# Kernel optimization log

Hardware: AMD Instinct MI355X
Metric: run time of the kernel (lower is better)

## Reference

```python
import jax, jax.numpy as jnp
import numpy as np

N, E = 30000, 180000
IN, H, OUT = 3000, 512, 30


def _segment_softmax(e, dst, n):
    # numerically stable softmax over incoming edges of each destination node
    m = jax.ops.segment_max(e, dst, num_segments=n)
    m = jnp.where(jnp.isfinite(m), m, 0.0)  # nodes with no in-edges
    ex = jnp.exp(e - m[dst])
    den = jax.ops.segment_sum(ex, dst, num_segments=n)
    return ex / den[dst]


def _gat(x, src, dst, Ws, Wd, a_s, a_d, n, alpha=None):
    """edGATConv (heads=1, no self-loops, no bias).
    xs = lin_s(x); attention score from lin_s(x)[src] and lin_d(x)[dst];
    out[i] = sum_{e: dst_e=i} alpha_e * xs[src_e].
    If alpha is given (tie_alpha), reuse it instead of recomputing."""
    xs = x @ Ws.T  # [n, F_out]
    if alpha is None:
        xd = x @ Wd.T
        e = jax.nn.leaky_relu(xs[src] @ a_s + xd[dst] @ a_d, 0.2)  # [E]
        alpha = _segment_softmax(e, dst, n)
    out = jax.ops.segment_sum(alpha[:, None] * xs[src], dst, num_segments=n)
    return out, alpha


def setup_inputs() -> dict:
    key = jax.random.key(0)
    ks = jax.random.split(key, 7)
    features = jax.random.normal(ks[0], (N, IN), dtype=jnp.float32)
    edge_index = jax.random.randint(ks[1], (2, E), 0, N)
    W1s = jax.random.normal(ks[2], (H, IN), dtype=jnp.float32) * 0.02
    W1d = jax.random.normal(ks[3], (H, IN), dtype=jnp.float32) * 0.02
    a1s = jax.random.normal(ks[4], (H,), dtype=jnp.float32) * 0.1
    a1d = jax.random.normal(ks[5], (H,), dtype=jnp.float32) * 0.1
    W2s = jax.random.normal(ks[6], (OUT, H), dtype=jnp.float32) * 0.05
    return {"features": features, "edge_index": edge_index,
            "W1s": W1s, "W1d": W1d, "a1s": a1s, "a1d": a1d, "W2s": W2s}


def reference(features, edge_index, W1s, W1d, a1s, a1d, W2s):
    src, dst = edge_index[0], edge_index[1]
    n = features.shape[0]
    # conv1: attentive GAT layer, stores tie_alpha
    h1, alpha1 = _gat(features, src, dst, W1s, W1d, a1s, a1d, n)
    h1 = jax.nn.elu(h1)
    # conv2: aslinear=True -> plain linear with lin_s
    h2 = h1 @ W2s.T  # [N, OUT]
    # conv3: weights tied to conv2 transposed, alpha tied to conv1
    # W3s = W2s.T so xs3 = h2 @ W3s.T = h2 @ W2s
    h3, _ = _gat(h2, src, dst, W2s.T, None, None, None, n, alpha=alpha1)
    h3 = jax.nn.elu(h3)
    # conv4: aslinear, weight tied to conv1 transposed: h3 @ W4s.T = h3 @ W1s
    h4 = h3 @ W1s  # [N, IN]
    return (h2, h4)
```

## Files before the change

kernel.cpp:

```cpp
#include <hip/hip_runtime.h>

typedef unsigned short u16;
typedef __bf16 bf16_t;
typedef bf16_t bf16x8 __attribute__((ext_vector_type(8)));
typedef float f32x4 __attribute__((ext_vector_type(4)));
typedef u16 u16x8 __attribute__((ext_vector_type(8)));

#define AS1 __attribute__((address_space(1)))
#define AS3 __attribute__((address_space(3)))

__device__ __forceinline__ u16 f2bf(float f) {
    union { float f; unsigned u; } v; v.f = f;
    unsigned r = v.u + 0x7FFFu + ((v.u >> 16) & 1u);
    return (u16)(r >> 16);
}
__device__ __forceinline__ float bf2f(u16 s) {
    union { unsigned u; float f; } v; v.u = ((unsigned)s) << 16;
    return v.f;
}

__device__ __forceinline__ void gload_lds16(const u16* g, u16* l) {
    __builtin_amdgcn_global_load_lds((AS1 const void*)g, (AS3 void*)l, 16, 0, 0);
}

template <bool OUT_BF16, bool GUARD>
__global__ __launch_bounds__(256) void gemm_bt(
    const u16* __restrict__ A, const u16* __restrict__ B, void* __restrict__ Cv,
    int K, int ldc, int Mreal, int Nreal, int vgx, int vgy)
{
    __shared__ u16 As[128 * 64];
    __shared__ u16 Bs[128 * 64];
    const int t = threadIdx.x;
    const int w = t >> 6, l = t & 63;
    const int wm = (w >> 1) * 64, wn = (w & 1) * 64;
    const int srow = w << 5;
    const int lrow = l >> 3, lc = l & 7;
    const int nwg = vgx * vgy;
    const int q = nwg >> 3, r = nwg & 7;

    for (int vb = blockIdx.x; vb < nwg; vb += gridDim.x) {
        const int xcd = vb & 7, loc = vb >> 3;
        const int swz = (xcd < r ? xcd * (q + 1) : r * (q + 1) + (xcd - r) * q) + loc;
        const int bx = swz % vgx, by = swz / vgx;
        const int m0 = by * 128, n0 = bx * 128;

        f32x4 acc[4][4] = {};

        for (int kt = 0; kt < K; kt += 64) {
#pragma unroll
            for (int i = 0; i < 4; ++i) {
                int row = srow + i * 8 + lrow;
                int gc = ((lc ^ (row & 7)) << 3);
                const u16* ga = A + (size_t)(m0 + row) * K + kt + gc;
                const u16* gb = B + (size_t)(n0 + row) * K + kt + gc;
                gload_lds16(ga, &As[(srow + i * 8) * 64]);
                gload_lds16(gb, &Bs[(srow + i * 8) * 64]);
            }
            asm volatile("s_waitcnt vmcnt(0)");
            __syncthreads();

#pragma unroll
            for (int kk = 0; kk < 2; ++kk) {
                bf16x8 af[4], bfr[4];
                int kc = kk * 4 + (l >> 4);
#pragma unroll
                for (int mi = 0; mi < 4; ++mi) {
                    int row = wm + mi * 16 + (l & 15);
                    af[mi] = *(const bf16x8*)&As[row * 64 + ((kc ^ (row & 7)) << 3)];
                }
#pragma unroll
                for (int ni = 0; ni < 4; ++ni) {
                    int col = wn + ni * 16 + (l & 15);
                    bfr[ni] = *(const bf16x8*)&Bs[col * 64 + ((kc ^ (col & 7)) << 3)];
                }
#pragma unroll
                for (int mi = 0; mi < 4; ++mi)
#pragma unroll
                    for (int ni = 0; ni < 4; ++ni)
                        acc[mi][ni] = __builtin_amdgcn_mfma_f32_16x16x32_bf16(
                            af[mi], bfr[ni], acc[mi][ni], 0, 0, 0);
            }
            __syncthreads();
        }

#pragma unroll
        for (int mi = 0; mi < 4; ++mi) {
#pragma unroll
            for (int qq = 0; qq < 4; ++qq) {
                int row = m0 + wm + mi * 16 + (l >> 4) * 4 + qq;
                if (GUARD && row >= Mreal) continue;
#pragma unroll
                for (int ni = 0; ni < 4; ++ni) {
                    int col = n0 + wn + ni * 16 + (l & 15);
                    if (GUARD && col >= Nreal) continue;
                    float v = acc[mi][ni][qq];
                    if (OUT_BF16) ((u16*)Cv)[(size_t)row * ldc + col] = f2bf(v);
                    else          ((float*)Cv)[(size_t)row * ldc + col] = v;
                }
            }
        }
    }
}

__global__ __launch_bounds__(256) void gemm_xw2(
    const float* __restrict__ X, const u16* __restrict__ Bw, u16* __restrict__ C,
    const float* __restrict__ vd, const float* __restrict__ vs,
    float* __restrict__ sd, float* __restrict__ ss)
{
    __shared__ u16 As[128 * 64];
    __shared__ u16 Bs[2][128 * 64];
    const int t = threadIdx.x;
    const int w = t >> 6, l = t & 63;
    const int wm = (w >> 1) * 64, wn = (w & 1) * 64;
    const int srow = w << 5;
    const int lrow = l >> 3, lc = l & 7;

    const int VGX = 4, NWG = 4 * 235;
    const int q = NWG >> 3, r = NWG & 7;

    for (int vb = blockIdx.x; vb < NWG; vb += gridDim.x) {
        const int xcd = vb & 7, loc = vb >> 3;
        const int swz = (xcd < r ? xcd * (q + 1) : r * (q + 1) + (xcd - r) * q) + loc;
        const int bx = swz % VGX, by = swz / VGX;
        const int m0 = by * 128, n0 = bx * 128;

        f32x4 acc[4][4] = {};
        float sdp[4] = {}, ssp[4] = {};
        const bool do_s = (bx == 0);

        int rowg[4];
        bool okr[4];
#pragma unroll
        for (int i = 0; i < 4; ++i) {
            rowg[i] = m0 + srow + i * 8 + lrow;
            okr[i] = rowg[i] < 30000;
        }

        float4 pa[4][2];
        auto loadA = [&](int kt) {
            int c = kt + lc * 8;
            bool okc = c < 3000;
#pragma unroll
            for (int i = 0; i < 4; ++i) {
                bool ok = okr[i] && okc;
                const float* p = X + (ok ? ((size_t)rowg[i] * 3000 + c) : 0);
                float4 v0 = *(const float4*)p;
                float4 v1 = *(const float4*)(p + 4);
                if (!ok) { v0 = make_float4(0.f, 0.f, 0.f, 0.f); v1 = v0; }
                pa[i][0] = v0;
                pa[i][1] = v1;
            }
        };
        auto stageB = [&](int kt2, int buf) {
#pragma unroll
            for (int i = 0; i < 4; ++i) {
                int row = srow + i * 8 + lrow;
                int gc = ((lc ^ (row & 7)) << 3);
                gload_lds16(Bw + (size_t)(n0 + row) * 3008 + kt2 + gc,
                            &Bs[buf][(srow + i * 8) * 64]);
            }
        };

        loadA(0);
        stageB(0, 0);
        int cur = 0;

        for (int kt = 0; kt < 3008; kt += 64) {
            if (do_s) {
                int c = kt + lc * 8;
                float4 d0 = *(const float4*)(vd + c);
                float4 d1 = *(const float4*)(vd + c + 4);
                float4 s0 = *(const float4*)(vs + c);
                float4 s1 = *(const float4*)(vs + c + 4);
#pragma unroll
                for (int i = 0; i < 4; ++i) {
                    sdp[i] += pa[i][0].x * d0.x + pa[i][0].y * d0.y + pa[i][0].z * d0.z + pa[i][0].w * d0.w
                            + pa[i][1].x * d1.x + pa[i][1].y * d1.y + pa[i][1].z * d1.z + pa[i][1].w * d1.w;
                    ssp[i] += pa[i][0].x * s0.x + pa[i][0].y * s0.y + pa[i][0].z * s0.z + pa[i][0].w * s0.w
                            + pa[i][1].x * s1.x + pa[i][1].y * s1.y + pa[i][1].z * s1.z + pa[i][1].w * s1.w;
                }
            }
#pragma unroll
            for (int i = 0; i < 4; ++i) {
                int row = srow + i * 8 + lrow;
                bf16x8 o;
                o[0] = (bf16_t)pa[i][0].x; o[1] = (bf16_t)pa[i][0].y;
                o[2] = (bf16_t)pa[i][0].z; o[3] = (bf16_t)pa[i][0].w;
                o[4] = (bf16_t)pa[i][1].x; o[5] = (bf16_t)pa[i][1].y;
                o[6] = (bf16_t)pa[i][1].z; o[7] = (bf16_t)pa[i][1].w;
                *(bf16x8*)&As[row * 64 + ((lc ^ (row & 7)) << 3)] = o;
            }
            loadA(kt + 64);
            int ktn = (kt + 64 < 3008) ? kt + 64 : 2944;
            stageB(ktn, cur ^ 1);
            asm volatile("s_waitcnt vmcnt(12) lgkmcnt(0)" ::: "memory");
            __builtin_amdgcn_s_barrier();

#pragma unroll
            for (int kk = 0; kk < 2; ++kk) {
                bf16x8 af[4], bfr[4];
                int kc = kk * 4 + (l >> 4);
#pragma unroll
                for (int mi = 0; mi < 4; ++mi) {
                    int row = wm + mi * 16 + (l & 15);
                    af[mi] = *(const bf16x8*)&As[row * 64 + ((kc ^ (row & 7)) << 3)];
                }
#pragma unroll
                for (int ni = 0; ni < 4; ++ni) {
                    int col = wn + ni * 16 + (l & 15);
                    bfr[ni] = *(const bf16x8*)&Bs[cur][col * 64 + ((kc ^ (col & 7)) << 3)];
                }
#pragma unroll
                for (int mi = 0; mi < 4; ++mi)
#pragma unroll
                    for (int ni = 0; ni < 4; ++ni)
                        acc[mi][ni] = __builtin_amdgcn_mfma_f32_16x16x32_bf16(
                            af[mi], bfr[ni], acc[mi][ni], 0, 0, 0);
            }
            asm volatile("s_barrier" ::: "memory");
            cur ^= 1;
        }

        if (do_s) {
#pragma unroll
            for (int i = 0; i < 4; ++i) {
                float a = sdp[i], b = ssp[i];
                a += __shfl_xor(a, 1); a += __shfl_xor(a, 2); a += __shfl_xor(a, 4);
                b += __shfl_xor(b, 1); b += __shfl_xor(b, 2); b += __shfl_xor(b, 4);
                if (lc == 0 && okr[i]) { sd[rowg[i]] = a; ss[rowg[i]] = b; }
            }
        }

#pragma unroll
        for (int mi = 0; mi < 4; ++mi)
#pragma unroll
            for (int qq = 0; qq < 4; ++qq) {
                int row = m0 + wm + mi * 16 + (l >> 4) * 4 + qq;
#pragma unroll
                for (int ni = 0; ni < 4; ++ni) {
                    int col = n0 + wn + ni * 16 + (l & 15);
                    C[(size_t)row * 512 + col] = f2bf(acc[mi][ni][qq]);
                }
            }
    }
}

__global__ void k_prep(const float* __restrict__ W1d, const float* __restrict__ a1d,
                       const float* __restrict__ W1s, const float* __restrict__ a1s,
                       const float* __restrict__ W2s, const int* __restrict__ dst,
                       float* __restrict__ vdp, float* __restrict__ vsp,
                       u16* __restrict__ w1sb, u16* __restrict__ w1st,
                       u16* __restrict__ w2sb, unsigned* __restrict__ deg) {
    int b = blockIdx.x, t = threadIdx.x;
    if (b < 48) {
        int hseg = b & 3, iblk = b >> 2;
        int i = iblk * 256 + t;
        if (i >= 3000) return;
        float ad = 0.f, as = 0.f;
        int h0 = hseg * 128;
        for (int h = h0; h < h0 + 128; ++h) {
            ad += W1d[(size_t)h * 3000 + i] * a1d[h];
            as += W1s[(size_t)h * 3000 + i] * a1s[h];
        }
        vdp[(size_t)hseg * 3008 + i] = ad;
        vsp[(size_t)hseg * 3008 + i] = as;
    } else if (b < 1552) {
        int idx = (b - 48) * 256 + t;
        int n = idx / 752, k = (idx % 752) * 4;
        ushort4 o = make_ushort4(0, 0, 0, 0);
        if (k < 3000) {
            float4 v = *(const float4*)(W1s + (size_t)n * 3000 + k);
            o.x = f2bf(v.x); o.y = f2bf(v.y); o.z = f2bf(v.z); o.w = f2bf(v.w);
        }
        *(ushort4*)(w1sb + (size_t)n * 3008 + k) = o;
    } else if (b < 1936) {
        __shared__ float tile[64][65];
        int fb = b - 1552;
        int i0 = (fb % 48) * 64, h0 = (fb / 48) * 64;
        int il = t & 63, hq = t >> 6;
#pragma unroll
        for (int rr = 0; rr < 16; ++rr) {
            int hl = rr * 4 + hq;
            int i = i0 + il;
            tile[hl][il] = (i < 3000) ? W1s[(size_t)(h0 + hl) * 3000 + i] : 0.f;
        }
        __syncthreads();
#pragma unroll
        for (int rr = 0; rr < 16; ++rr) {
            int il2 = rr * 4 + hq;
            w1st[(size_t)(i0 + il2) * 512 + h0 + il] = f2bf(tile[il][il2]);
        }
    } else if (b < 2192) {
        int idx = (b - 1936) * 256 + t;
        int n = idx >> 9, k = idx & 511;
        w2sb[idx] = (n < 30) ? f2bf(W2s[(size_t)n * 512 + k]) : (u16)0;
    } else {
        int j = (b - 2192) * 256 + t;
        if (j < 180000) atomicAdd(&deg[dst[j]], 1u);
    }
}

__global__ void k_comb_scan1(const float* __restrict__ vdp, const float* __restrict__ vsp,
                             float* __restrict__ vd, float* __restrict__ vs,
                             const unsigned* __restrict__ deg, unsigned* __restrict__ bsum,
                             int n) {
    int b = blockIdx.x, t = threadIdx.x;
    if (b < 12) {
        int i = b * 256 + t;
        if (i >= 3008) return;
        if (i < 3000) {
            vd[i] = vdp[i] + vdp[3008 + i] + vdp[6016 + i] + vdp[9024 + i];
            vs[i] = vsp[i] + vsp[3008 + i] + vsp[6016 + i] + vsp[9024 + i];
        } else {
            vd[i] = 0.f;
            vs[i] = 0.f;
        }
    } else {
        __shared__ unsigned ws[4];
        int bb = b - 12;
        int i = bb * 256 + t;
        unsigned v = (i < n) ? deg[i] : 0u;
#pragma unroll
        for (int s = 32; s; s >>= 1) v += __shfl_xor(v, s);
        if ((t & 63) == 0) ws[t >> 6] = v;
        __syncthreads();
        if (t == 0) bsum[bb] = ws[0] + ws[1] + ws[2] + ws[3];
    }
}

__global__ void k_scanB(const unsigned* __restrict__ deg, const unsigned* __restrict__ bsum,
                        unsigned* __restrict__ off, unsigned* __restrict__ cur,
                        int n, int nb) {
    __shared__ unsigned tmp[256];
    __shared__ unsigned bo;
    int b = blockIdx.x, t = threadIdx.x, i = b * 256 + t;
    if (t < 64) {
        unsigned s0 = (t < nb) ? bsum[t] : 0u;
        unsigned s1 = (t + 64 < nb) ? bsum[t + 64] : 0u;
        unsigned v = ((t < b) ? s0 : 0u) + ((t + 64 < b) ? s1 : 0u);
#pragma unroll
        for (int s = 32; s; s >>= 1) v += __shfl_xor(v, s);
        if (t == 0) bo = v;
        if (b == nb - 1) {
            unsigned tv = s0 + s1;
#pragma unroll
            for (int s = 32; s; s >>= 1) tv += __shfl_xor(tv, s);
            if (t == 0) off[n] = tv;
        }
    }
    __syncthreads();
    unsigned v = (i < n) ? deg[i] : 0u;
    tmp[t] = v;
    __syncthreads();
    for (int s = 1; s < 256; s <<= 1) {
        unsigned a = (t >= s) ? tmp[t - s] : 0u;
        __syncthreads();
        tmp[t] += a;
        __syncthreads();
    }
    if (i < n) {
        unsigned o = bo + tmp[t] - v;
        off[i] = o;
        cur[i] = o;
    }
}

__global__ void k_fill(const int* __restrict__ dst, unsigned* __restrict__ cur,
                       unsigned* __restrict__ csr) {
    int j = blockIdx.x * 256 + threadIdx.x;
    if (j >= 180000) return;
    unsigned pos = atomicAdd(&cur[dst[j]], 1u);
    csr[pos] = (unsigned)j;
}

__global__ void k_soft(const int* __restrict__ src, const float* __restrict__ ss,
                       const float* __restrict__ sd, float* __restrict__ alpha,
                       const unsigned* __restrict__ csr, const unsigned* __restrict__ off) {
    int t = threadIdx.x;
    int g = t >> 3, l = t & 7;
    int n = blockIdx.x * 32 + g;
    if (n >= 30000) return;
    unsigned lo = off[n], hi = off[n + 1];
    if (lo == hi) return;
    float sdn = sd[n];
    float m = -1e30f;
    for (unsigned i = lo + l; i < hi; i += 8) {
        float v = ss[src[csr[i]]] + sdn;
        v = v > 0.f ? v : 0.2f * v;
        m = fmaxf(m, v);
    }
    m = fmaxf(m, __shfl_xor(m, 1));
    m = fmaxf(m, __shfl_xor(m, 2));
    m = fmaxf(m, __shfl_xor(m, 4));
    float den = 0.f;
    for (unsigned i = lo + l; i < hi; i += 8) {
        float v = ss[src[csr[i]]] + sdn;
        v = v > 0.f ? v : 0.2f * v;
        den += expf(v - m);
    }
    den += __shfl_xor(den, 1);
    den += __shfl_xor(den, 2);
    den += __shfl_xor(den, 4);
    float inv = 1.f / den;
    for (unsigned i = lo + l; i < hi; i += 8) {
        unsigned j = csr[i];
        float v = ss[src[j]] + sdn;
        v = v > 0.f ? v : 0.2f * v;
        alpha[j] = expf(v - m) * inv;
    }
}

__global__ void k_agg(const u16* __restrict__ xin, const float* __restrict__ alpha,
                      const unsigned* __restrict__ csr, const unsigned* __restrict__ off,
                      const int* __restrict__ src, u16* __restrict__ outb, int nvalid) {
    int w = threadIdx.x >> 6, l = threadIdx.x & 63;
    int n = blockIdx.x * 4 + w;
    float acc[8] = {};
    if (n < nvalid) {
        unsigned lo = off[n], hi = off[n + 1];
        unsigned i = lo;
        for (; i + 2 <= hi; i += 2) {
            unsigned j0 = csr[i], j1 = csr[i + 1];
            float a0 = alpha[j0], a1 = alpha[j1];
            int s0 = src[j0], s1 = src[j1];
            u16x8 r0 = *(const u16x8*)&xin[(size_t)s0 * 512 + l * 8];
            u16x8 r1 = *(const u16x8*)&xin[(size_t)s1 * 512 + l * 8];
#pragma unroll
            for (int k = 0; k < 8; ++k) acc[k] += a0 * bf2f(r0[k]) + a1 * bf2f(r1[k]);
        }
        if (i < hi) {
            unsigned j0 = csr[i];
            float a0 = alpha[j0];
            int s0 = src[j0];
            u16x8 r0 = *(const u16x8*)&xin[(size_t)s0 * 512 + l * 8];
#pragma unroll
            for (int k = 0; k < 8; ++k) acc[k] += a0 * bf2f(r0[k]);
        }
    }
    u16x8 o;
#pragma unroll
    for (int k = 0; k < 8; ++k) {
        float a = acc[k] > 0.f ? acc[k] : expf(acc[k]) - 1.f;
        o[k] = f2bf(a);
    }
    *(u16x8*)&outb[(size_t)n * 512 + l * 8] = o;
}

__global__ void k_aggh3(const float* __restrict__ h2, const float* __restrict__ alpha,
                        const unsigned* __restrict__ csr, const unsigned* __restrict__ off,
                        const int* __restrict__ src, const float* __restrict__ W2s,
                        u16* __restrict__ h3b) {
    __shared__ float gs[8][32];
    int t = threadIdx.x;
    int grp = t >> 5, c = t & 31;
    size_t n0 = (size_t)blockIdx.x * 8;
    int n = (int)n0 + grp;
    float acc = 0.f;
    if (n < 30000 && c < 30) {
        unsigned lo = off[n], hi = off[n + 1];
        for (unsigned i = lo; i < hi; ++i) {
            unsigned j = csr[i];
            acc += alpha[j] * h2[(size_t)src[j] * 30 + c];
        }
    }
    gs[grp][c] = acc;
    __syncthreads();

    float w0[30], w1[30];
#pragma unroll
    for (int o = 0; o < 30; ++o) {
        w0[o] = W2s[(size_t)o * 512 + t];
        w1[o] = W2s[(size_t)o * 512 + t + 256];
    }
    for (int rr = 0; rr < 8; ++rr) {
        const float* gr = gs[rr];
        float a0 = 0.f, a1 = 0.f;
#pragma unroll
        for (int o = 0; o < 30; ++o) {
            float v = gr[o];
            a0 += v * w0[o];
            a1 += v * w1[o];
        }
        a0 = a0 > 0.f ? a0 : expf(a0) - 1.f;
        a1 = a1 > 0.f ? a1 : expf(a1) - 1.f;
        size_t nn = n0 + rr;
        h3b[nn * 512 + t] = f2bf(a0);
        h3b[nn * 512 + t + 256] = f2bf(a1);
    }
}

extern "C" void kernel_launch(void* const* d_in, const int* in_sizes, int n_in,
                              void* d_out, int out_size, void* d_ws, size_t ws_size,
                              hipStream_t stream) {
    const float* X   = (const float*)d_in[0];
    const int*   ei  = (const int*)d_in[1];
    const float* W1s = (const float*)d_in[2];
    const float* W1d = (const float*)d_in[3];
    const float* a1s = (const float*)d_in[4];
    const float* a1d = (const float*)d_in[5];
    const float* W2s = (const float*)d_in[6];
    const int* src = ei;
    const int* dst = ei + 180000;

    float* out = (float*)d_out;
    float* h2 = out;
    float* h4 = out + 900000;

    char* ob = (char*)(out + 900000);
    u16* xs1b = (u16*)ob;
    u16* h1b  = (u16*)(ob + 30801920);

    char* w = (char*)d_ws;
    auto carve = [&](size_t bytes) { char* p = w; w += (bytes + 255) & ~(size_t)255; return p; };
    u16* w1sb  = (u16*)carve((size_t)512 * 3008 * 2);
    u16* w1st  = (u16*)carve((size_t)3072 * 512 * 2);
    u16* w2sb  = (u16*)carve((size_t)128 * 512 * 2);
    u16* h3b   = (u16*)carve((size_t)30080 * 512 * 2);
    float* vd    = (float*)carve(3008 * 4);
    float* vs    = (float*)carve(3008 * 4);
    float* vdp   = (float*)carve(4 * 3008 * 4);
    float* vsp   = (float*)carve(4 * 3008 * 4);
    float* ss    = (float*)carve(30000 * 4);
    float* sd    = (float*)carve(30000 * 4);
    float* alpha = (float*)carve(180000 * 4);
    unsigned* deg = (unsigned*)carve(30000 * 4);
    unsigned* off = (unsigned*)carve(30004 * 4);
    unsigned* cur = (unsigned*)carve(30000 * 4);
    unsigned* csr = (unsigned*)carve(180000 * 4);
    unsigned* bsum = (unsigned*)carve(128 * 4);

    hipMemsetAsync(deg, 0, 30000 * 4, stream);

    k_prep<<<2896, 256, 0, stream>>>(W1d, a1d, W1s, a1s, W2s, dst,
                                     vdp, vsp, w1sb, w1st, w2sb, deg);
    k_comb_scan1<<<130, 256, 0, stream>>>(vdp, vsp, vd, vs, deg, bsum, 30000);

    gemm_xw2<<<768, 256, 0, stream>>>(X, w1sb, xs1b, vd, vs, sd, ss);

    k_scanB<<<118, 256, 0, stream>>>(deg, bsum, off, cur, 30000, 118);
    k_fill<<<704, 256, 0, stream>>>(dst, cur, csr);
    k_soft<<<938, 256, 0, stream>>>(src, ss, sd, alpha, csr, off);

    k_agg <<<7520, 256, 0, stream>>>(xs1b, alpha, csr, off, src, h1b, 30000);

    gemm_bt<false, true><<<235, 256, 0, stream>>>(h1b, w2sb, h2, 512, 30, 30000, 30, 1, 235);

    k_aggh3<<<3760, 256, 0, stream>>>(h2, alpha, csr, off, src, W2s, h3b);

    gemm_bt<false, true><<<1280, 256, 0, stream>>>(h3b, w1st, h4, 512, 3000, 30000, 3000, 24, 235);
}
```

Baseline: 594.1 us.

## Fuse layer-1 aggregation, ELU and W2s projection into one kernel

The edge aggregation kernel now applies ELU and immediately projects each node's 512-wide hidden vector onto the 30 output channels. It uses W2s staged in LDS and a wave-level butterfly reduction, writing h2 directly. This removes the bf16 h1 round trip through memory and the separate small GEMM launch. In exchange, each block loads 30 KB of weights into LDS, and each wave does 30 six-step shuffle reductions, which adds register pressure and may lower occupancy.

```diff
diff --git a/kernel.cpp b/kernel.cpp
--- a/kernel.cpp
+++ b/kernel.cpp
@@ -410,13 +410,21 @@
     }
 }
 
-__global__ void k_agg(const u16* __restrict__ xin, const float* __restrict__ alpha,
-                      const unsigned* __restrict__ csr, const unsigned* __restrict__ off,
-                      const int* __restrict__ src, u16* __restrict__ outb, int nvalid) {
-    int w = threadIdx.x >> 6, l = threadIdx.x & 63;
+__global__ __launch_bounds__(256) void k_aggh2(
+    const u16* __restrict__ xin, const float* __restrict__ alpha,
+    const unsigned* __restrict__ csr, const unsigned* __restrict__ off,
+    const int* __restrict__ src, const u16* __restrict__ w2sb,
+    float* __restrict__ h2) {
+    __shared__ u16 w2l[30 * 512];
+    int t = threadIdx.x;
+    for (int i = t; i < 1920; i += 256)
+        *(u16x8*)&w2l[i * 8] = *(const u16x8*)&w2sb[i * 8];
+    __syncthreads();
+
+    int w = t >> 6, l = t & 63;
     int n = blockIdx.x * 4 + w;
-    float acc[8] = {};
-    if (n < nvalid) {
+    float a[8] = {};
+    if (n < 30000) {
         unsigned lo = off[n], hi = off[n + 1];
         unsigned i = lo;
         for (; i + 2 <= hi; i += 2) {
@@ -426,7 +434,7 @@
             u16x8 r0 = *(const u16x8*)&xin[(size_t)s0 * 512 + l * 8];
             u16x8 r1 = *(const u16x8*)&xin[(size_t)s1 * 512 + l * 8];
 #pragma unroll
-            for (int k = 0; k < 8; ++k) acc[k] += a0 * bf2f(r0[k]) + a1 * bf2f(r1[k]);
+            for (int k = 0; k < 8; ++k) a[k] += a0 * bf2f(r0[k]) + a1 * bf2f(r1[k]);
         }
         if (i < hi) {
             unsigned j0 = csr[i];
@@ -434,16 +442,30 @@
             int s0 = src[j0];
             u16x8 r0 = *(const u16x8*)&xin[(size_t)s0 * 512 + l * 8];
 #pragma unroll
-            for (int k = 0; k < 8; ++k) acc[k] += a0 * bf2f(r0[k]);
-        }
-    }
-    u16x8 o;
-#pragma unroll
-    for (int k = 0; k < 8; ++k) {
-        float a = acc[k] > 0.f ? acc[k] : expf(acc[k]) - 1.f;
-        o[k] = f2bf(a);
-    }
-    *(u16x8*)&outb[(size_t)n * 512 + l * 8] = o;
+            for (int k = 0; k < 8; ++k) a[k] += a0 * bf2f(r0[k]);
+        }
+    }
+#pragma unroll
+    for (int k = 0; k < 8; ++k) a[k] = a[k] > 0.f ? a[k] : expf(a[k]) - 1.f;
+
+    float part[30];
+#pragma unroll
+    for (int o = 0; o < 30; ++o) {
+        bf16x8 wr = *(const bf16x8*)&w2l[o * 512 + l * 8];
+        float p = 0.f;
+#pragma unroll
+        for (int k = 0; k < 8; ++k) p += a[k] * (float)wr[k];
+        part[o] = p;
+    }
+#pragma unroll
+    for (int s = 1; s <= 32; s <<= 1) {
+#pragma unroll
+        for (int o = 0; o < 30; ++o) part[o] += __shfl_xor(part[o], s);
+    }
+    if (l == 0 && n < 30000) {
+#pragma unroll
+        for (int o = 0; o < 30; ++o) h2[(size_t)n * 30 + o] = part[o];
+    }
 }
 
 __global__ void k_aggh3(const float* __restrict__ h2, const float* __restrict__ alpha,
@@ -508,7 +530,6 @@
 
     char* ob = (char*)(out + 900000);
     u16* xs1b = (u16*)ob;
-    u16* h1b  = (u16*)(ob + 30801920);
 
     char* w = (char*)d_ws;
     auto carve = [&](size_t bytes) { char* p = w; w += (bytes + 255) & ~(size_t)255; return p; };
@@ -541,9 +562,7 @@
     k_fill<<<704, 256, 0, stream>>>(dst, cur, csr);
     k_soft<<<938, 256, 0, stream>>>(src, ss, sd, alpha, csr, off);
 
-    k_agg <<<7520, 256, 0, stream>>>(xs1b, alpha, csr, off, src, h1b, 30000);
-
-    gemm_bt<false, true><<<235, 256, 0, stream>>>(h1b, w2sb, h2, 512, 30, 30000, 30, 1, 235);
+    k_aggh2<<<7500, 256, 0, stream>>>(xs1b, alpha, csr, off, src, w2sb, h2);
 
     k_aggh3<<<3760, 256, 0, stream>>>(h2, alpha, csr, off, src, W2s, h3b);
 
```

New measurement: 670.7 us. +12.9%, slower.
